# Optimization experiments

Measured on AMD Instinct MI355X. Metric: run time of the kernel, lower is better.

Reference implementation:

```python
import jax, jax.numpy as jnp
import numpy as np

N = 100_000   # nodes
E = 1_600_000 # edges
V = 100_000   # vocab
G = 256       # graphs in batch
D = 64        # emb/hidden dim


def setup_inputs() -> dict:
    key = jax.random.key(0)
    ks = jax.random.split(key, 12)
    x_tokens = jax.random.randint(ks[0], (N, 1), 0, V)
    edge_index = jax.random.randint(ks[1], (2, E), 0, N)
    batch = jnp.sort(jax.random.randint(ks[2], (N,), 0, G))
    s = 0.02
    return {
        "x_tokens": x_tokens,
        "edge_index": edge_index,
        "batch": batch,
        "emb_table": jax.random.normal(ks[3], (V, D), jnp.float32) * s,
        "W0": jax.random.normal(ks[4], (D, D), jnp.float32) * s,
        "b0": jnp.zeros((D,), jnp.float32),
        "W1": jax.random.normal(ks[5], (D, D), jnp.float32) * s,
        "b1": jnp.zeros((D,), jnp.float32),
        "W2": jax.random.normal(ks[6], (D, D), jnp.float32) * s,
        "b2": jnp.zeros((D,), jnp.float32),
        "Wc1": jax.random.normal(ks[7], (2 * D, D), jnp.float32) * s,
        "bc1": jnp.zeros((D,), jnp.float32),
        "Wc2": jax.random.normal(ks[8], (D, 2), jnp.float32) * s,
        "bc2": jnp.zeros((2,), jnp.float32),
    }


def _gcn_norm(edge_index, n_nodes):
    # add self loops, compute symmetric normalization coefficients
    loop = jnp.arange(n_nodes, dtype=edge_index.dtype)
    src = jnp.concatenate([edge_index[0], loop])
    dst = jnp.concatenate([edge_index[1], loop])
    deg = jax.ops.segment_sum(jnp.ones_like(dst, jnp.float32), dst, num_segments=n_nodes)
    dinv = jnp.where(deg > 0, deg ** -0.5, 0.0)
    norm = dinv[src] * dinv[dst]  # [E+N]
    return src, dst, norm


def _gcn_conv(x, W, b, src, dst, norm, n_nodes):
    x = x @ W                                   # [N, D]
    msg = x[src] * norm[:, None]                # gather + scale, [E+N, D]
    out = jax.ops.segment_sum(msg, dst, num_segments=n_nodes)
    return out + b


def reference(x_tokens, edge_index, batch, emb_table, W0, b0, W1, b1, W2, b2, Wc1, bc1, Wc2, bc2):
    n = x_tokens.shape[0]
    src, dst, norm = _gcn_norm(edge_index, n)
    x = emb_table[x_tokens[:, 0]]               # [N, D]
    for W, b in ((W0, b0), (W1, b1), (W2, b2)):
        x = jax.nn.relu(_gcn_conv(x, W, b, src, dst, norm, n))
    # dual pooling over graph ids
    cnt = jax.ops.segment_sum(jnp.ones((n,), x.dtype), batch, num_segments=G)
    h_sum = jax.ops.segment_sum(x, batch, num_segments=G)
    h_mean = h_sum / jnp.maximum(cnt, 1.0)[:, None]
    h_max = jax.ops.segment_max(x, batch, num_segments=G)
    h_max = jnp.where(jnp.isfinite(h_max), h_max, 0.0)
    h = jnp.concatenate([h_mean, h_max], axis=-1)   # [G, 2D]
    logits = jax.nn.relu(h @ Wc1 + bc1) @ Wc2 + bc2  # [G, 2]
    return logits
```

## Files before the change

### kernel.cpp

```cpp
#include <hip/hip_runtime.h>
#include <hip/hip_fp16.h>
#include <math.h>


#define BKT_LOG 9
#define BKT (1 << BKT_LOG)
#define CHUNK 4096

typedef _Float16 h2 __attribute__((ext_vector_type(2)));
typedef _Float16 f16x8 __attribute__((ext_vector_type(8)));
typedef float f32x4 __attribute__((ext_vector_type(4)));

union HU { unsigned u; h2 h; };
__device__ inline h2 h2bits(unsigned u) { HU x; x.u = u; return x.h; }

#if __has_builtin(__builtin_amdgcn_fdot2)
#define FDOT2(a, b, c) __builtin_amdgcn_fdot2((a), (b), (c), false)
#else
__device__ inline float FDOT2(h2 a, h2 b, float c) {
  return (float)a.x * (float)b.x + (float)a.y * (float)b.y + c;
}
#endif

#define MASK_X 0x00003C00u
#define MASK_Y 0x3C000000u

__device__ inline void acc8c(const uint4& v, float* acc) {
  const unsigned* w = (const unsigned*)&v;
#pragma unroll
  for (int k = 0; k < 4; k++) {
    h2 hv = h2bits(w[k]);
    acc[2 * k]     = FDOT2(hv, h2bits(MASK_X), acc[2 * k]);
    acc[2 * k + 1] = FDOT2(hv, h2bits(MASK_Y), acc[2 * k + 1]);
  }
}

__global__ __launch_bounds__(256) void k_wcvt(const float* __restrict__ W0,
                                              const float* __restrict__ W1,
                                              const float* __restrict__ W2,
                                              _Float16* __restrict__ Wf,
                                              int* __restrict__ chist,
                                              float* __restrict__ hz, int hzn) {
  if (blockIdx.x < 3) {
    const float* W = (blockIdx.x == 0) ? W0 : (blockIdx.x == 1) ? W1 : W2;
    _Float16* out = Wf + blockIdx.x * 4096;
    for (int i = threadIdx.x; i < 4096; i += 256) {
      int c = i >> 10, s = (i >> 9) & 1, l = (i >> 3) & 63, j = i & 7;
      int k = 32 * s + 8 * (l >> 4) + j;
      int ncol = 16 * c + (l & 15);
      out[i] = (_Float16)W[k * 64 + ncol];
    }
  } else if (blockIdx.x == 3) {
    chist[threadIdx.x] = 0;
  } else {
    for (int i = threadIdx.x; i < hzn; i += 256) hz[i] = 0.f;
  }
}

__global__ __launch_bounds__(256) void k_chist(const int* __restrict__ dst,
                                               int* __restrict__ chist, int E, int B) {
  __shared__ int h[256];
  h[threadIdx.x] = 0;
  __syncthreads();
  for (long e = (long)blockIdx.x * blockDim.x + threadIdx.x; e < E;
       e += (long)gridDim.x * blockDim.x)
    atomicAdd(&h[dst[e] >> BKT_LOG], 1);
  __syncthreads();
  if (threadIdx.x < B && h[threadIdx.x]) atomicAdd(&chist[threadIdx.x], h[threadIdx.x]);
}

__global__ __launch_bounds__(256) void k_cscan(const int* __restrict__ chist,
                                               int* __restrict__ cbase,
                                               int* __restrict__ gcur, int E, int B) {
  __shared__ int s[256];
  int v = (threadIdx.x < B) ? chist[threadIdx.x] : 0;
  s[threadIdx.x] = v;
  __syncthreads();
  for (int d = 1; d < 256; d <<= 1) {
    int t = (threadIdx.x >= (unsigned)d) ? s[threadIdx.x - d] : 0;
    __syncthreads();
    s[threadIdx.x] += t;
    __syncthreads();
  }
  if (threadIdx.x < B) {
    int ex = s[threadIdx.x] - v;
    cbase[threadIdx.x] = ex;
    gcur[threadIdx.x] = ex;
  }
  if (threadIdx.x == B) cbase[B] = E;
}

__global__ __launch_bounds__(256) void k_part(const int* __restrict__ src,
                                              const int* __restrict__ dst,
                                              int* __restrict__ gcur,
                                              int* __restrict__ ebuf, int E, int B) {
  __shared__ int sA[CHUNK];
  __shared__ int dA[CHUNK];
  __shared__ int h[256], base[256];
  int tid = threadIdx.x;
  long c0 = (long)blockIdx.x * CHUNK;
  int m = (int)min((long)CHUNK, (long)E - c0);
  h[tid] = 0;
  __syncthreads();
  for (int i = tid; i < m; i += 256) {
    int s = src[c0 + i];
    int d = dst[c0 + i];
    sA[i] = s;
    dA[i] = d;
    atomicAdd(&h[d >> BKT_LOG], 1);
  }
  __syncthreads();
  if (tid < B && h[tid]) base[tid] = atomicAdd(&gcur[tid], h[tid]);
  __syncthreads();
  h[tid] = 0;
  __syncthreads();
  for (int i = tid; i < m; i += 256) {
    int s = sA[i], d = dA[i];
    int k = d >> BKT_LOG;
    int p = base[k] + atomicAdd(&h[k], 1);
    ebuf[p] = ((d & (BKT - 1)) << 17) | s;
  }
}

__global__ __launch_bounds__(512) void k_bplace(const int* __restrict__ ebuf,
                                                const int* __restrict__ cbase,
                                                int* __restrict__ off,
                                                int* __restrict__ csrc,
                                                float* __restrict__ dinv,
                                                int N, int E) {
  __shared__ int s[512];
  __shared__ int cur[512];
  int b = blockIdx.x, tid = threadIdx.x;
  int n0 = b << BKT_LOG;
  int nn = min(BKT, N - n0);
  int e0 = cbase[b], e1 = cbase[b + 1];
  s[tid] = 0;
  __syncthreads();
  for (int e = e0 + tid; e < e1; e += 512) atomicAdd(&s[ebuf[e] >> 17], 1);
  __syncthreads();
  int deg = s[tid];
  for (int d = 1; d < 512; d <<= 1) {
    int t = (tid >= d) ? s[tid - d] : 0;
    __syncthreads();
    s[tid] += t;
    __syncthreads();
  }
  int excl = s[tid] - deg;
  if (tid < nn) {
    off[n0 + tid] = e0 + excl;
    dinv[n0 + tid] = 1.0f / sqrtf((float)(1 + deg));
  }
  cur[tid] = excl;
  __syncthreads();
  for (int e = e0 + tid; e < e1; e += 512) {
    int p = ebuf[e];
    int pos = e0 + atomicAdd(&cur[p >> 17], 1);
    csrc[pos] = p & 0x1FFFF;
  }
  if (b == 0 && tid == 0) off[N] = E;
}

template <bool EMB>
__global__ __launch_bounds__(256) void k_mfmamm(const _Float16* __restrict__ y,
                                                const int* __restrict__ tok,
                                                const float* __restrict__ emb,
                                                const _Float16* __restrict__ Wf,
                                                const float* __restrict__ dinv,
                                                float scale,
                                                _Float16* __restrict__ xh,
                                                int n, int npad) {
  __shared__ _Float16 lds[4 * 16 * 72];
  int w = threadIdx.x >> 6, l = threadIdx.x & 63;
  int m = l & 15, q = l >> 4;
  int rbase = blockIdx.x * 64 + w * 16;

  f16x8 a0, a1;
  if (EMB) {
    int node = min(rbase + m, n - 1);
    const float* er = emb + (size_t)tok[node] * 64;
    float4 v0 = *(const float4*)(er + q * 8);
    float4 v1 = *(const float4*)(er + q * 8 + 4);
    float4 v2 = *(const float4*)(er + 32 + q * 8);
    float4 v3 = *(const float4*)(er + 32 + q * 8 + 4);
    a0[0] = (_Float16)v0.x; a0[1] = (_Float16)v0.y; a0[2] = (_Float16)v0.z; a0[3] = (_Float16)v0.w;
    a0[4] = (_Float16)v1.x; a0[5] = (_Float16)v1.y; a0[6] = (_Float16)v1.z; a0[7] = (_Float16)v1.w;
    a1[0] = (_Float16)v2.x; a1[1] = (_Float16)v2.y; a1[2] = (_Float16)v2.z; a1[3] = (_Float16)v2.w;
    a1[4] = (_Float16)v3.x; a1[5] = (_Float16)v3.y; a1[6] = (_Float16)v3.z; a1[7] = (_Float16)v3.w;
  } else {
    int node = rbase + m;
    a0 = *(const f16x8*)(y + ((size_t)(q >> 1) * npad + node) * 16 + (q & 1) * 8);
    a1 = *(const f16x8*)(y + ((size_t)((q >> 1) + 2) * npad + node) * 16 + (q & 1) * 8);
  }
  float4 d4 = *(const float4*)(dinv + rbase + q * 4);

  const f16x8* wf = (const f16x8*)Wf + l;
  f32x4 acc[4];
#pragma unroll
  for (int c = 0; c < 4; c++) {
    f32x4 z = {0.f, 0.f, 0.f, 0.f};
    z = __builtin_amdgcn_mfma_f32_16x16x32_f16(a0, wf[(c * 2 + 0) * 64], z, 0, 0, 0);
    z = __builtin_amdgcn_mfma_f32_16x16x32_f16(a1, wf[(c * 2 + 1) * 64], z, 0, 0, 0);
    acc[c] = z;
  }

  const float ds[4] = {d4.x * scale, d4.y * scale, d4.z * scale, d4.w * scale};
  _Float16* ldw = lds + w * 16 * 72;
#pragma unroll
  for (int c = 0; c < 4; c++)
#pragma unroll
    for (int r = 0; r < 4; r++)
      ldw[(q * 4 + r) * 72 + c * 16 + m] = (_Float16)(acc[c][r] * ds[r]);
  __syncthreads();

  int row2 = l & 15, c2 = l >> 4;
  int node = rbase + row2;
  if (node < n) {
    const uint4* s4 = (const uint4*)(ldw + row2 * 72 + c2 * 16);
    uint4 v0 = s4[0], v1 = s4[1];
    uint4* dst = (uint4*)(xh + ((size_t)c2 * npad + node) * 16);
    dst[0] = v0;
    dst[1] = v1;
  }
}

__global__ __launch_bounds__(256) void k_aggregate(const int* __restrict__ off,
                                                   const int* __restrict__ csrc,
                                                   const float* __restrict__ dinv,
                                                   const _Float16* __restrict__ xh,
                                                   const float* __restrict__ bias,
                                                   _Float16* __restrict__ outp,
                                                   int n, int npad) {
  int c = blockIdx.x & 3;
  int lane = threadIdx.x & 63;
  int n4 = lane >> 4, g = (lane >> 1) & 7, o = lane & 1;
  int t = (blockIdx.x >> 2) * 16 + (threadIdx.x >> 6) * 4 + n4;
  bool valid = t < n;
  int tc = valid ? t : n - 1;
  int e0 = off[tc], e1 = off[tc + 1];
  if (!valid) e1 = e0;
  const uint4* x4 = (const uint4*)xh + (size_t)c * npad * 2;

  float acc[8];
#pragma unroll
  for (int k = 0; k < 8; k++) acc[k] = 0.f;
  if (g == 0) acc8c(x4[(size_t)tc * 2 + o], acc);

  int iA = e0 + g;
  bool aA = iA < e1, aB = iA + 8 < e1;
  int sA = aA ? csrc[iA] : 0;
  int sB = aB ? csrc[iA + 8] : 0;
  while (aA) {
    uint4 vA = x4[(size_t)sA * 2 + o];
    uint4 vB;
    if (aB) vB = x4[(size_t)sB * 2 + o];
    int iN = iA + 16;
    bool aN = iN < e1, aM = iN + 8 < e1;
    int sN = 0, sM = 0;
    if (aN) sN = csrc[iN];
    if (aM) sM = csrc[iN + 8];
    acc8c(vA, acc);
    if (aB) acc8c(vB, acc);
    iA = iN; aA = aN; sA = sN;
    aB = aM; sB = sM;
  }

#pragma unroll
  for (int mm = 2; mm <= 8; mm <<= 1) {
#pragma unroll
    for (int k = 0; k < 8; k++) acc[k] += __shfl_xor(acc[k], mm);
  }

  if (valid && g == 0) {
    float sc = dinv[t] * (1.0f / 256.0f);
    int f0 = c * 16 + o * 8;
    float4 bb0 = *(const float4*)(bias + f0);
    float4 bb1 = *(const float4*)(bias + f0 + 4);
    const float bs[8] = {bb0.x, bb0.y, bb0.z, bb0.w, bb1.x, bb1.y, bb1.z, bb1.w};
    _Float16 hh[8];
#pragma unroll
    for (int k = 0; k < 8; k++)
      hh[k] = (_Float16)(fmaxf(acc[k] * sc + bs[k], 0.f) * 4096.f);
    *(uint4*)(outp + ((size_t)c * npad + t) * 16 + o * 8) = *(const uint4*)hh;
  }
}

__global__ __launch_bounds__(256) void k_pool(const _Float16* __restrict__ x,
                                              const int* __restrict__ batch,
                                              float* __restrict__ hsum,
                                              float* __restrict__ hmax,
                                              int* __restrict__ cntg,
                                              int n, int npad) {
  int wid = (blockIdx.x * blockDim.x + threadIdx.x) >> 6;
  int lane = threadIdx.x & 63;
  int i0 = wid * 64;
  if (i0 >= n) return;
  int i1 = min(i0 + 64, n);
  size_t sb = (size_t)(lane >> 4) * npad * 16 + (lane & 15);
  int batch_l = (i0 + lane < n) ? batch[i0 + lane] : 0;
  float gsum = 0.f, gmax = 0.f;
  int cur = __shfl(batch_l, 0);
  int c = 0;
  for (int i = i0; i < i1; i++) {
    int g = __shfl(batch_l, i - i0);
    if (g != cur) {
      atomicAdd(&hsum[cur * 64 + lane], gsum);
      atomicMax((int*)&hmax[cur * 64 + lane], __float_as_int(gmax));
      if (lane == 0) atomicAdd(&cntg[cur], c);
      gsum = 0.f; gmax = 0.f; c = 0; cur = g;
    }
    float v = (float)x[sb + (size_t)i * 16];
    gsum += v;
    gmax = fmaxf(gmax, v);
    c++;
  }
  atomicAdd(&hsum[cur * 64 + lane], gsum);
  atomicMax((int*)&hmax[cur * 64 + lane], __float_as_int(gmax));
  if (lane == 0) atomicAdd(&cntg[cur], c);
}

__global__ __launch_bounds__(64) void k_cls(const float* __restrict__ hsum,
                                            const float* __restrict__ hmax,
                                            const int* __restrict__ cnt,
                                            const float* __restrict__ Wc1,
                                            const float* __restrict__ bc1,
                                            const float* __restrict__ Wc2,
                                            const float* __restrict__ bc2,
                                            float* __restrict__ out) {
  __shared__ float h[128];
  __shared__ float hid[64];
  int g = blockIdx.x, j = threadIdx.x;
  int c = cnt[g];
  float cf = (float)(c > 0 ? c : 1);
  h[j] = hsum[g * 64 + j] / cf * (1.0f / 4096.0f);
  h[64 + j] = hmax[g * 64 + j] * (1.0f / 4096.0f);
  __syncthreads();
  float acc = bc1[j];
  for (int k = 0; k < 128; k++) acc += h[k] * Wc1[k * 64 + j];
  hid[j] = fmaxf(acc, 0.f);
  __syncthreads();
  if (j < 2) {
    float a = bc2[j];
    for (int k = 0; k < 64; k++) a += hid[k] * Wc2[k * 2 + j];
    out[g * 2 + j] = a;
  }
}

extern "C" void kernel_launch(void* const* d_in, const int* in_sizes, int n_in,
                              void* d_out, int out_size, void* d_ws, size_t ws_size,
                              hipStream_t stream) {
  const int N = in_sizes[0];
  const int E = in_sizes[1] / 2;
  const int G = out_size / 2;
  const int B = (N + BKT - 1) >> BKT_LOG;
  const int Npad = (N + 63) & ~63;

  const int* tok   = (const int*)d_in[0];
  const int* ei    = (const int*)d_in[1];
  const int* batch = (const int*)d_in[2];
  const float* emb = (const float*)d_in[3];
  const float* W0 = (const float*)d_in[4];  const float* b0 = (const float*)d_in[5];
  const float* W1 = (const float*)d_in[6];  const float* b1 = (const float*)d_in[7];
  const float* W2 = (const float*)d_in[8];  const float* b2 = (const float*)d_in[9];
  const float* Wc1 = (const float*)d_in[10]; const float* bc1 = (const float*)d_in[11];
  const float* Wc2 = (const float*)d_in[12]; const float* bc2 = (const float*)d_in[13];
  const int* srcp = ei;
  const int* dstp = ei + E;

  int* off    = (int*)d_ws;
  int* csrc   = off + N + 2;
  float* dinv = (float*)(csrc + E);
  int* chist  = (int*)(dinv + Npad);
  int* cbase  = chist + 256;
  int* gcur   = cbase + 256;
  _Float16* Wf = (_Float16*)(gcur + 256);
  _Float16* xh = Wf + 3 * 4096;
  _Float16* y  = xh + (size_t)Npad * 64;
  int* ebuf   = (int*)(y + (size_t)Npad * 64);
  float* hsum = (float*)(ebuf + E);
  float* hmax = hsum + (size_t)G * 64;
  int*   cntg = (int*)(hmax + (size_t)G * 64);

  auto cdiv = [](long a, long b) { return (int)((a + b - 1) / b); };
  const int aggBlocks = 4 * cdiv(N, 16);

  k_wcvt<<<5, 256, 0, stream>>>(W0, W1, W2, Wf, chist, hsum, G * 129);

  k_chist<<<cdiv(E, CHUNK), 256, 0, stream>>>(dstp, chist, E, B);
  k_cscan<<<1, 256, 0, stream>>>(chist, cbase, gcur, E, B);
  k_part<<<cdiv(E, CHUNK), 256, 0, stream>>>(srcp, dstp, gcur, ebuf, E, B);
  k_bplace<<<B, 512, 0, stream>>>(ebuf, cbase, off, csrc, dinv, N, E);

  k_mfmamm<true><<<cdiv(N, 64), 256, 0, stream>>>(nullptr, tok, emb, Wf, dinv, 256.f, xh, N, Npad);
  k_aggregate<<<aggBlocks, 256, 0, stream>>>(off, csrc, dinv, xh, b0, y, N, Npad);

  k_mfmamm<false><<<cdiv(N, 64), 256, 0, stream>>>(y, nullptr, nullptr, Wf + 4096, dinv, 1.f / 16.f, xh, N, Npad);
  k_aggregate<<<aggBlocks, 256, 0, stream>>>(off, csrc, dinv, xh, b1, y, N, Npad);

  k_mfmamm<false><<<cdiv(N, 64), 256, 0, stream>>>(y, nullptr, nullptr, Wf + 8192, dinv, 1.f / 16.f, xh, N, Npad);
  k_aggregate<<<aggBlocks, 256, 0, stream>>>(off, csrc, dinv, xh, b2, y, N, Npad);

  k_pool<<<cdiv(N, 256), 256, 0, stream>>>(y, batch, hsum, hmax, cntg, N, Npad);

  k_cls<<<G, 64, 0, stream>>>(hsum, hmax, cntg, Wc1, bc1, Wc2, bc2, (float*)d_out);
}
```

Baseline: 366.0 us.

## Replace bucket histogram+scan with fixed-capacity per-bucket slots in CSR build

```diff
diff --git a/kernel.cpp b/kernel.cpp
--- a/kernel.cpp
+++ b/kernel.cpp
@@ -39,7 +39,7 @@
                                               const float* __restrict__ W1,
                                               const float* __restrict__ W2,
                                               _Float16* __restrict__ Wf,
-                                              int* __restrict__ chist,
+                                              int* __restrict__ gcur,
                                               float* __restrict__ hz, int hzn) {
   if (blockIdx.x < 3) {
     const float* W = (blockIdx.x == 0) ? W0 : (blockIdx.x == 1) ? W1 : W2;
@@ -51,49 +51,17 @@
       out[i] = (_Float16)W[k * 64 + ncol];
     }
   } else if (blockIdx.x == 3) {
-    chist[threadIdx.x] = 0;
+    gcur[threadIdx.x] = 0;
   } else {
     for (int i = threadIdx.x; i < hzn; i += 256) hz[i] = 0.f;
   }
-}
-
-__global__ __launch_bounds__(256) void k_chist(const int* __restrict__ dst,
-                                               int* __restrict__ chist, int E, int B) {
-  __shared__ int h[256];
-  h[threadIdx.x] = 0;
-  __syncthreads();
-  for (long e = (long)blockIdx.x * blockDim.x + threadIdx.x; e < E;
-       e += (long)gridDim.x * blockDim.x)
-    atomicAdd(&h[dst[e] >> BKT_LOG], 1);
-  __syncthreads();
-  if (threadIdx.x < B && h[threadIdx.x]) atomicAdd(&chist[threadIdx.x], h[threadIdx.x]);
-}
-
-__global__ __launch_bounds__(256) void k_cscan(const int* __restrict__ chist,
-                                               int* __restrict__ cbase,
-                                               int* __restrict__ gcur, int E, int B) {
-  __shared__ int s[256];
-  int v = (threadIdx.x < B) ? chist[threadIdx.x] : 0;
-  s[threadIdx.x] = v;
-  __syncthreads();
-  for (int d = 1; d < 256; d <<= 1) {
-    int t = (threadIdx.x >= (unsigned)d) ? s[threadIdx.x - d] : 0;
-    __syncthreads();
-    s[threadIdx.x] += t;
-    __syncthreads();
-  }
-  if (threadIdx.x < B) {
-    int ex = s[threadIdx.x] - v;
-    cbase[threadIdx.x] = ex;
-    gcur[threadIdx.x] = ex;
-  }
-  if (threadIdx.x == B) cbase[B] = E;
 }
 
 __global__ __launch_bounds__(256) void k_part(const int* __restrict__ src,
                                               const int* __restrict__ dst,
                                               int* __restrict__ gcur,
-                                              int* __restrict__ ebuf, int E, int B) {
+                                              int* __restrict__ ebuf,
+                                              int E, int S) {
   __shared__ int sA[CHUNK];
   __shared__ int dA[CHUNK];
   __shared__ int h[256], base[256];
@@ -110,7 +78,7 @@
     atomicAdd(&h[d >> BKT_LOG], 1);
   }
   __syncthreads();
-  if (tid < B && h[tid]) base[tid] = atomicAdd(&gcur[tid], h[tid]);
+  if (h[tid]) base[tid] = atomicAdd(&gcur[tid], h[tid]);
   __syncthreads();
   h[tid] = 0;
   __syncthreads();
@@ -118,25 +86,28 @@
     int s = sA[i], d = dA[i];
     int k = d >> BKT_LOG;
     int p = base[k] + atomicAdd(&h[k], 1);
-    ebuf[p] = ((d & (BKT - 1)) << 17) | s;
+    if (p < S)
+      ebuf[k * S + p] = ((d & (BKT - 1)) << 17) | s;
   }
 }
 
 __global__ __launch_bounds__(512) void k_bplace(const int* __restrict__ ebuf,
-                                                const int* __restrict__ cbase,
+                                                const int* __restrict__ gcur,
                                                 int* __restrict__ off,
+                                                int* __restrict__ eend,
                                                 int* __restrict__ csrc,
                                                 float* __restrict__ dinv,
-                                                int N, int E) {
+                                                int N, int S) {
   __shared__ int s[512];
   __shared__ int cur[512];
   int b = blockIdx.x, tid = threadIdx.x;
   int n0 = b << BKT_LOG;
   int nn = min(BKT, N - n0);
-  int e0 = cbase[b], e1 = cbase[b + 1];
+  int e0 = b * S;
+  int cnt = min(gcur[b], S);
   s[tid] = 0;
   __syncthreads();
-  for (int e = e0 + tid; e < e1; e += 512) atomicAdd(&s[ebuf[e] >> 17], 1);
+  for (int e = tid; e < cnt; e += 512) atomicAdd(&s[ebuf[e0 + e] >> 17], 1);
   __syncthreads();
   int deg = s[tid];
   for (int d = 1; d < 512; d <<= 1) {
@@ -148,16 +119,16 @@
   int excl = s[tid] - deg;
   if (tid < nn) {
     off[n0 + tid] = e0 + excl;
+    eend[n0 + tid] = e0 + excl + deg;
     dinv[n0 + tid] = 1.0f / sqrtf((float)(1 + deg));
   }
   cur[tid] = excl;
   __syncthreads();
-  for (int e = e0 + tid; e < e1; e += 512) {
-    int p = ebuf[e];
+  for (int e = tid; e < cnt; e += 512) {
+    int p = ebuf[e0 + e];
     int pos = e0 + atomicAdd(&cur[p >> 17], 1);
     csrc[pos] = p & 0x1FFFF;
   }
-  if (b == 0 && tid == 0) off[N] = E;
 }
 
 template <bool EMB>
@@ -224,6 +195,7 @@
 }
 
 __global__ __launch_bounds__(256) void k_aggregate(const int* __restrict__ off,
+                                                   const int* __restrict__ eend,
                                                    const int* __restrict__ csrc,
                                                    const float* __restrict__ dinv,
                                                    const _Float16* __restrict__ xh,
@@ -236,7 +208,7 @@
   int t = (blockIdx.x >> 2) * 16 + (threadIdx.x >> 6) * 4 + n4;
   bool valid = t < n;
   int tc = valid ? t : n - 1;
-  int e0 = off[tc], e1 = off[tc + 1];
+  int e0 = off[tc], e1 = eend[tc];
   if (!valid) e1 = e0;
   const uint4* x4 = (const uint4*)xh + (size_t)c * npad * 2;
 
@@ -353,6 +325,7 @@
   const int G = out_size / 2;
   const int B = (N + BKT - 1) >> BKT_LOG;
   const int Npad = (N + 63) & ~63;
+  const int S = ((((E + B - 1) / B) * 3 / 2 + 256) + 3) & ~3;
 
   const int* tok   = (const int*)d_in[0];
   const int* ei    = (const int*)d_in[1];
@@ -367,37 +340,34 @@
   const int* dstp = ei + E;
 
   int* off    = (int*)d_ws;
-  int* csrc   = off + N + 2;
-  float* dinv = (float*)(csrc + E);
-  int* chist  = (int*)(dinv + Npad);
-  int* cbase  = chist + 256;
-  int* gcur   = cbase + 256;
+  int* eend   = off + N;
+  float* dinv = (float*)(eend + N);
+  int* gcur   = (int*)(dinv + Npad);
   _Float16* Wf = (_Float16*)(gcur + 256);
-  _Float16* xh = Wf + 3 * 4096;
+  int* csrc   = (int*)(Wf + 3 * 4096);
+  _Float16* xh = (_Float16*)(csrc + (size_t)B * S);
   _Float16* y  = xh + (size_t)Npad * 64;
-  int* ebuf   = (int*)(y + (size_t)Npad * 64);
-  float* hsum = (float*)(ebuf + E);
+  int* ebuf   = (int*)y;
+  float* hsum = (float*)(y + (size_t)Npad * 64);
   float* hmax = hsum + (size_t)G * 64;
   int*   cntg = (int*)(hmax + (size_t)G * 64);
 
   auto cdiv = [](long a, long b) { return (int)((a + b - 1) / b); };
   const int aggBlocks = 4 * cdiv(N, 16);
 
-  k_wcvt<<<5, 256, 0, stream>>>(W0, W1, W2, Wf, chist, hsum, G * 129);
-
-  k_chist<<<cdiv(E, CHUNK), 256, 0, stream>>>(dstp, chist, E, B);
-  k_cscan<<<1, 256, 0, stream>>>(chist, cbase, gcur, E, B);
-  k_part<<<cdiv(E, CHUNK), 256, 0, stream>>>(srcp, dstp, gcur, ebuf, E, B);
-  k_bplace<<<B, 512, 0, stream>>>(ebuf, cbase, off, csrc, dinv, N, E);
+  k_wcvt<<<5, 256, 0, stream>>>(W0, W1, W2, Wf, gcur, hsum, G * 129);
+
+  k_part<<<cdiv(E, CHUNK), 256, 0, stream>>>(srcp, dstp, gcur, ebuf, E, S);
+  k_bplace<<<B, 512, 0, stream>>>(ebuf, gcur, off, eend, csrc, dinv, N, S);
 
   k_mfmamm<true><<<cdiv(N, 64), 256, 0, stream>>>(nullptr, tok, emb, Wf, dinv, 256.f, xh, N, Npad);
-  k_aggregate<<<aggBlocks, 256, 0, stream>>>(off, csrc, dinv, xh, b0, y, N, Npad);
+  k_aggregate<<<aggBlocks, 256, 0, stream>>>(off, eend, csrc, dinv, xh, b0, y, N, Npad);
 
   k_mfmamm<false><<<cdiv(N, 64), 256, 0, stream>>>(y, nullptr, nullptr, Wf + 4096, dinv, 1.f / 16.f, xh, N, Npad);
-  k_aggregate<<<aggBlocks, 256, 0, stream>>>(off, csrc, dinv, xh, b1, y, N, Npad);
+  k_aggregate<<<aggBlocks, 256, 0, stream>>>(off, eend, csrc, dinv, xh, b1, y, N, Npad);
 
   k_mfmamm<false><<<cdiv(N, 64), 256, 0, stream>>>(y, nullptr, nullptr, Wf + 8192, dinv, 1.f / 16.f, xh, N, Npad);
-  k_aggregate<<<aggBlocks, 256, 0, stream>>>(off, csrc, dinv, xh, b2, y, N, Npad);
+  k_aggregate<<<aggBlocks, 256, 0, stream>>>(off, eend, csrc, dinv, xh, b2, y, N, Npad);
 
   k_pool<<<cdiv(N, 256), 256, 0, stream>>>(y, batch, hsum, hmax, cntg, N, Npad);
 
```

After: 333.2 us (median of 2 runs). 1.1x faster.
